# Kernel optimization log

Hardware: AMD Instinct MI355X
Metric: run time of the kernel (lower is better)

The kernel has to match this reference:

```python
import jax, jax.numpy as jnp
import numpy as np

H = 128

def _rnn_layer(inp, W_ih, W_hh, b_ih, b_hh):
    # inp: [B, T, D]; precompute the input projection for all timesteps at once
    pre = jnp.einsum('btd,hd->bth', inp, W_ih) + b_ih + b_hh  # [B, T, H]
    B = inp.shape[0]
    h0 = jnp.zeros((B, H), dtype=inp.dtype)

    def step(h, p_t):  # p_t: [B, H]
        h_new = jnp.tanh(p_t + h @ W_hh.T)
        return h_new, h_new

    _, hs = jax.lax.scan(step, h0, jnp.swapaxes(pre, 0, 1))  # [T, B, H]
    return jnp.swapaxes(hs, 0, 1)  # [B, T, H]


def setup_inputs() -> dict:
    key = jax.random.key(0)
    ks = jax.random.split(key, 12)
    B, T, D = 64, 512, 2048
    s_in = 1.0 / np.sqrt(H)  # PyTorch RNN init scale ~ U(-1/sqrt(H), 1/sqrt(H))
    u = lambda k, shape: jax.random.uniform(k, shape, jnp.float32, -s_in, s_in)
    return {
        'x': jax.random.normal(ks[0], (B, T, D), jnp.float32),
        'W_ih1': u(ks[1], (H, D)),
        'W_hh1': u(ks[2], (H, H)),
        'b_ih1': u(ks[3], (H,)),
        'b_hh1': u(ks[4], (H,)),
        'W_ih2': u(ks[5], (H, H)),
        'W_hh2': u(ks[6], (H, H)),
        'b_ih2': u(ks[7], (H,)),
        'b_hh2': u(ks[8], (H,)),
        'W_fc': u(ks[9], (1, H)),
        'b_fc': u(ks[10], (1,)),
    }


def reference(x, W_ih1, W_hh1, b_ih1, b_hh1, W_ih2, W_hh2, b_ih2, b_hh2, W_fc, b_fc):
    h1 = _rnn_layer(x, W_ih1, W_hh1, b_ih1, b_hh1)   # [B, T, H]
    h2 = _rnn_layer(h1, W_ih2, W_hh2, b_ih2, b_hh2)  # [B, T, H]
    last = h2[:, -1, :]                               # [B, H]
    return last @ W_fc.T + b_fc                       # [B, 1]
```

## Files before the change

### kernel.cpp

```cpp
#include <hip/hip_runtime.h>
#include <cstddef>
#include <cstdint>

#define BB 64
#define TT 512
#define DD 2048
#define HH 128
#define M1 (BB*TT)

typedef __attribute__((ext_vector_type(8))) short bf16x8;
typedef __attribute__((ext_vector_type(4))) float f32x4;
typedef __attribute__((ext_vector_type(2))) _Float16 h2f;

__device__ __forceinline__ unsigned short f2bf(float f) {
    unsigned u = __builtin_bit_cast(unsigned, f);
    u += 0x7fffu + ((u >> 16) & 1u);
    return (unsigned short)(u >> 16);
}
__device__ __forceinline__ float bf2f(unsigned short s) {
    return __builtin_bit_cast(float, ((unsigned)s) << 16);
}
__device__ __forceinline__ float tanh_fast(float x) {
    float e2x = __builtin_amdgcn_exp2f(x * 2.885390081777927f);
    return 1.0f - 2.0f * __builtin_amdgcn_rcpf(e2x + 1.0f);
}

__global__ __launch_bounds__(256) void prep_w_kernel(
    const float* __restrict__ W,
    unsigned short* __restrict__ Whi, unsigned short* __restrict__ Wlo)
{
    const int i = (blockIdx.x * 256 + threadIdx.x) * 4;
    float4 w = *(const float4*)(W + i);
    unsigned short h0 = f2bf(w.x), h1 = f2bf(w.y), h2 = f2bf(w.z), h3 = f2bf(w.w);
    unsigned short l0 = f2bf(w.x - bf2f(h0)), l1 = f2bf(w.y - bf2f(h1));
    unsigned short l2 = f2bf(w.z - bf2f(h2)), l3 = f2bf(w.w - bf2f(h3));
    ushort4 hv; hv.x = h0; hv.y = h1; hv.z = h2; hv.w = h3;
    ushort4 lv; lv.x = l0; lv.y = l1; lv.z = l2; lv.w = l3;
    *(ushort4*)(Whi + i) = hv;
    *(ushort4*)(Wlo + i) = lv;
}

__global__ __launch_bounds__(256) void gemm1_mfma_kernel(
    const float* __restrict__ A, const unsigned short* __restrict__ Whi,
    const unsigned short* __restrict__ Wlo,
    const float* __restrict__ bia, const float* __restrict__ bib,
    float* __restrict__ out)
{
    constexpr int K = DD, BK = 32, NK = K / BK;
    __shared__ __align__(16) short Ah[64 * 40];
    __shared__ __align__(16) short Al[64 * 40];
    __shared__ __align__(16) short Wh[128 * 40];
    __shared__ __align__(16) short Wl[128 * 40];

    const int tid = threadIdx.x, wave = tid >> 6, lane = tid & 63;
    const size_t m0 = (size_t)blockIdx.x * 64;
    const int ar = tid >> 2, ak = (tid & 3) * 8;
    const int wr = tid >> 1, wk = (tid & 1) * 16;
    const float* Ap = A + (m0 + ar) * (size_t)K + ak;
    const unsigned short* Whp = Whi + (size_t)wr * K + wk;
    const unsigned short* Wlp = Wlo + (size_t)wr * K + wk;
    const int frow = lane & 15, fko = (lane >> 4) * 8;

    f32x4 acc[8];
#pragma unroll
    for (int i = 0; i < 8; i++) acc[i] = (f32x4){0.f, 0.f, 0.f, 0.f};

    for (int kt = 0; kt < NK; ++kt) {
        float4 a0 = *(const float4*)(Ap + kt * BK);
        float4 a1 = *(const float4*)(Ap + kt * BK + 4);
        bf16x8 wh0 = *(const bf16x8*)(Whp + kt * BK);
        bf16x8 wh1 = *(const bf16x8*)(Whp + kt * BK + 8);
        bf16x8 wl0 = *(const bf16x8*)(Wlp + kt * BK);
        bf16x8 wl1 = *(const bf16x8*)(Wlp + kt * BK + 8);
        __syncthreads();
        float fv[8] = {a0.x, a0.y, a0.z, a0.w, a1.x, a1.y, a1.z, a1.w};
        unsigned short h[8], l[8];
#pragma unroll
        for (int i = 0; i < 8; i++) {
            h[i] = f2bf(fv[i]);
            l[i] = f2bf(fv[i] - bf2f(h[i]));
        }
        uint2 p0, p1, q0, q1;
        p0.x = (unsigned)h[0] | ((unsigned)h[1] << 16); p0.y = (unsigned)h[2] | ((unsigned)h[3] << 16);
        p1.x = (unsigned)h[4] | ((unsigned)h[5] << 16); p1.y = (unsigned)h[6] | ((unsigned)h[7] << 16);
        q0.x = (unsigned)l[0] | ((unsigned)l[1] << 16); q0.y = (unsigned)l[2] | ((unsigned)l[3] << 16);
        q1.x = (unsigned)l[4] | ((unsigned)l[5] << 16); q1.y = (unsigned)l[6] | ((unsigned)l[7] << 16);
        *(uint2*)&Ah[ar * 40 + ak]     = p0;
        *(uint2*)&Ah[ar * 40 + ak + 4] = p1;
        *(uint2*)&Al[ar * 40 + ak]     = q0;
        *(uint2*)&Al[ar * 40 + ak + 4] = q1;
        *(bf16x8*)&Wh[wr * 40 + wk]     = wh0;
        *(bf16x8*)&Wh[wr * 40 + wk + 8] = wh1;
        *(bf16x8*)&Wl[wr * 40 + wk]     = wl0;
        *(bf16x8*)&Wl[wr * 40 + wk + 8] = wl1;
        __syncthreads();
        bf16x8 fAh = *(const bf16x8*)&Ah[(wave * 16 + frow) * 40 + fko];
        bf16x8 fAl = *(const bf16x8*)&Al[(wave * 16 + frow) * 40 + fko];
#pragma unroll
        for (int nt = 0; nt < 8; ++nt) {
            bf16x8 fWh = *(const bf16x8*)&Wh[(nt * 16 + frow) * 40 + fko];
            bf16x8 fWl = *(const bf16x8*)&Wl[(nt * 16 + frow) * 40 + fko];
            acc[nt] = __builtin_amdgcn_mfma_f32_16x16x32_bf16(fAh, fWh, acc[nt], 0, 0, 0);
            acc[nt] = __builtin_amdgcn_mfma_f32_16x16x32_bf16(fAh, fWl, acc[nt], 0, 0, 0);
            acc[nt] = __builtin_amdgcn_mfma_f32_16x16x32_bf16(fAl, fWh, acc[nt], 0, 0, 0);
        }
    }
    const int rbase = (lane >> 4) * 4;
#pragma unroll
    for (int nt = 0; nt < 8; ++nt) {
        const int col = nt * 16 + frow;
        const float bv = bia[col] + bib[col];
#pragma unroll
        for (int r = 0; r < 4; r++)
            out[(m0 + wave * 16 + rbase + r) * HH + col] = acc[nt][r] + bv;
    }
}

__global__ __launch_bounds__(256, 1) void rnn_scan4_fused1(
    const float* __restrict__ pre,
    const float* __restrict__ Whh,
    const float* __restrict__ Wih2,
    const float* __restrict__ bi2, const float* __restrict__ bh2,
    float* __restrict__ pre2)
{
    __shared__ __align__(16) _Float16 hs[2][HH];
    const int tid  = threadIdx.x;
    const int wave = tid >> 6, lane = tid & 63;
    const int j  = wave * 32 + (lane & 31);
    const int kh = lane >> 5;
    const int b  = blockIdx.x;

    h2f Wr[32];
    h2f W2r[32];
    {
        const float* r = Whh + (size_t)j * HH + kh * 64;
        const float* r2 = Wih2 + (size_t)j * HH + kh * 64;
#pragma unroll
        for (int q = 0; q < 16; q++) {
            float4 w = *(const float4*)(r + q * 4);
            Wr[2 * q]     = h2f{(_Float16)w.x, (_Float16)w.y};
            Wr[2 * q + 1] = h2f{(_Float16)w.z, (_Float16)w.w};
            float4 v = *(const float4*)(r2 + q * 4);
            W2r[2 * q]     = h2f{(_Float16)v.x, (_Float16)v.y};
            W2r[2 * q + 1] = h2f{(_Float16)v.z, (_Float16)v.w};
        }
    }
    const float bias2 = bi2[j] + bh2[j];
    if (tid < HH) hs[0][tid] = (_Float16)0.f;

    const float* pb = pre + (size_t)b * TT * HH;
    float* p2b = pre2 + (size_t)b * TT * HH;
    float pn0 = pb[j];
    float pn1 = pb[(size_t)HH + j];
    __syncthreads();

    for (int t = 0; t < TT; ++t) {
        const float p = pn0;
        pn0 = pn1;
        if (t + 2 < TT) pn1 = pb[(size_t)(t + 2) * HH + j];
        const int rb = t & 1;
        const int wb = rb ^ 1;
        const _Float16* hp = &hs[rb][kh * 64];
        float a0 = 0.f, a1 = 0.f, a2 = 0.f, a3 = 0.f;
#pragma unroll
        for (int q = 0; q < 8; q++) {
            uint4 hv = *(const uint4*)(hp + q * 8);
            h2f x0 = __builtin_bit_cast(h2f, hv.x);
            h2f x1 = __builtin_bit_cast(h2f, hv.y);
            h2f x2 = __builtin_bit_cast(h2f, hv.z);
            h2f x3 = __builtin_bit_cast(h2f, hv.w);
            a0 = __builtin_amdgcn_fdot2(Wr[4 * q],     x0, a0, false);
            a1 = __builtin_amdgcn_fdot2(Wr[4 * q + 1], x1, a1, false);
            a2 = __builtin_amdgcn_fdot2(Wr[4 * q + 2], x2, a2, false);
            a3 = __builtin_amdgcn_fdot2(Wr[4 * q + 3], x3, a3, false);
        }
        float s = (a0 + a1) + (a2 + a3);
        s += __shfl_xor(s, 32);
        const float h = tanh_fast(p + s);
        if (lane < 32) hs[wb][j] = (_Float16)h;
        __syncthreads();

        const _Float16* h2p = &hs[wb][kh * 64];
        float c0 = 0.f, c1 = 0.f, c2 = 0.f, c3 = 0.f;
#pragma unroll
        for (int q = 0; q < 8; q++) {
            uint4 hv = *(const uint4*)(h2p + q * 8);
            h2f x0 = __builtin_bit_cast(h2f, hv.x);
            h2f x1 = __builtin_bit_cast(h2f, hv.y);
            h2f x2 = __builtin_bit_cast(h2f, hv.z);
            h2f x3 = __builtin_bit_cast(h2f, hv.w);
            c0 = __builtin_amdgcn_fdot2(W2r[4 * q],     x0, c0, false);
            c1 = __builtin_amdgcn_fdot2(W2r[4 * q + 1], x1, c1, false);
            c2 = __builtin_amdgcn_fdot2(W2r[4 * q + 2], x2, c2, false);
            c3 = __builtin_amdgcn_fdot2(W2r[4 * q + 3], x3, c3, false);
        }
        float s2 = (c0 + c1) + (c2 + c3);
        s2 += __shfl_xor(s2, 32);
        if (lane < 32) p2b[(size_t)t * HH + j] = s2 + bias2;
    }
}

__global__ __launch_bounds__(256, 1) void rnn_scan4_final(
    const float* __restrict__ pre,
    const float* __restrict__ Whh,
    const float* __restrict__ Wfc, const float* __restrict__ bfc,
    float* __restrict__ outv)
{
    __shared__ __align__(16) _Float16 hs[2][HH];
    __shared__ float red[4];
    const int tid  = threadIdx.x;
    const int wave = tid >> 6, lane = tid & 63;
    const int j  = wave * 32 + (lane & 31);
    const int kh = lane >> 5;
    const int b  = blockIdx.x;

    h2f Wr[32];
    {
        const float* r = Whh + (size_t)j * HH + kh * 64;
#pragma unroll
        for (int q = 0; q < 16; q++) {
            float4 w = *(const float4*)(r + q * 4);
            Wr[2 * q]     = h2f{(_Float16)w.x, (_Float16)w.y};
            Wr[2 * q + 1] = h2f{(_Float16)w.z, (_Float16)w.w};
        }
    }
    if (tid < HH) hs[0][tid] = (_Float16)0.f;

    const float* pb = pre + (size_t)b * TT * HH;
    float pn0 = pb[j];
    float pn1 = pb[(size_t)HH + j];
    float fcv = 0.f;
    __syncthreads();

    for (int t = 0; t < TT; ++t) {
        const float p = pn0;
        pn0 = pn1;
        if (t + 2 < TT) pn1 = pb[(size_t)(t + 2) * HH + j];
        const int rb = t & 1;
        const int wb = rb ^ 1;
        const _Float16* hp = &hs[rb][kh * 64];
        float a0 = 0.f, a1 = 0.f, a2 = 0.f, a3 = 0.f;
#pragma unroll
        for (int q = 0; q < 8; q++) {
            uint4 hv = *(const uint4*)(hp + q * 8);
            h2f x0 = __builtin_bit_cast(h2f, hv.x);
            h2f x1 = __builtin_bit_cast(h2f, hv.y);
            h2f x2 = __builtin_bit_cast(h2f, hv.z);
            h2f x3 = __builtin_bit_cast(h2f, hv.w);
            a0 = __builtin_amdgcn_fdot2(Wr[4 * q],     x0, a0, false);
            a1 = __builtin_amdgcn_fdot2(Wr[4 * q + 1], x1, a1, false);
            a2 = __builtin_amdgcn_fdot2(Wr[4 * q + 2], x2, a2, false);
            a3 = __builtin_amdgcn_fdot2(Wr[4 * q + 3], x3, a3, false);
        }
        float s = (a0 + a1) + (a2 + a3);
        s += __shfl_xor(s, 32);
        const float h = tanh_fast(p + s);
        if (lane < 32) hs[wb][j] = (_Float16)h;
        if (t == TT - 1 && lane < 32) fcv = h * Wfc[j];
        __syncthreads();
    }

#pragma unroll
    for (int off = 1; off < 64; off <<= 1) fcv += __shfl_xor(fcv, off);
    if (lane == 0) red[wave] = fcv;
    __syncthreads();
    if (tid == 0) outv[b] = red[0] + red[1] + red[2] + red[3] + bfc[0];
}

extern "C" void kernel_launch(void* const* d_in, const int* in_sizes, int n_in,
                              void* d_out, int out_size, void* d_ws, size_t ws_size,
                              hipStream_t stream) {
    const float* x    = (const float*)d_in[0];
    const float* Wih1 = (const float*)d_in[1];
    const float* Whh1 = (const float*)d_in[2];
    const float* bih1 = (const float*)d_in[3];
    const float* bhh1 = (const float*)d_in[4];
    const float* Wih2 = (const float*)d_in[5];
    const float* Whh2 = (const float*)d_in[6];
    const float* bih2 = (const float*)d_in[7];
    const float* bhh2 = (const float*)d_in[8];
    const float* Wfc  = (const float*)d_in[9];
    const float* bfc  = (const float*)d_in[10];
    float* out = (float*)d_out;

    float* preA = (float*)d_ws;
    float* preB = preA + (size_t)M1 * HH;
    unsigned short* Whi = (unsigned short*)preB;
    unsigned short* Wlo = Whi + (size_t)HH * DD;

    prep_w_kernel<<<dim3(HH * DD / 1024), dim3(256), 0, stream>>>(Wih1, Whi, Wlo);
    gemm1_mfma_kernel<<<dim3(M1 / 64), dim3(256), 0, stream>>>(x, Whi, Wlo, bih1, bhh1, preA);
    rnn_scan4_fused1<<<dim3(BB), dim3(256), 0, stream>>>(
        preA, Whh1, Wih2, bih2, bhh2, preB);
    rnn_scan4_final<<<dim3(BB), dim3(256), 0, stream>>>(
        preB, Whh2, Wfc, bfc, out);
}
```

Baseline: 882.8 us.

## Split fused scan into producer and consumer waves for layer-2 projection

The fused layer-1 kernel now runs 8 waves per block. Four waves perform the recurrent scan, and four compute the layer-2 input projection for the previous timestep in parallel. This removes the second serial dot product and the extra barrier from each step's critical path, at the cost of a doubled block size and a one-step skew with a tail step after the loop. Weight loading is moved into a helper with an asm register pin so the weights stay resident in registers. The launch bounds no longer force one block per CU.

```diff
diff --git a/kernel.cpp b/kernel.cpp
--- a/kernel.cpp
+++ b/kernel.cpp
@@ -23,6 +23,38 @@
 __device__ __forceinline__ float tanh_fast(float x) {
     float e2x = __builtin_amdgcn_exp2f(x * 2.885390081777927f);
     return 1.0f - 2.0f * __builtin_amdgcn_rcpf(e2x + 1.0f);
+}
+
+__device__ __forceinline__ float dot64_f16(const h2f* Wr, const _Float16* hp) {
+    float a0 = 0.f, a1 = 0.f, a2 = 0.f, a3 = 0.f;
+#pragma unroll
+    for (int q = 0; q < 8; q++) {
+        uint4 hv = *(const uint4*)(hp + q * 8);
+        h2f x0 = __builtin_bit_cast(h2f, hv.x);
+        h2f x1 = __builtin_bit_cast(h2f, hv.y);
+        h2f x2 = __builtin_bit_cast(h2f, hv.z);
+        h2f x3 = __builtin_bit_cast(h2f, hv.w);
+        a0 = __builtin_amdgcn_fdot2(Wr[4 * q],     x0, a0, false);
+        a1 = __builtin_amdgcn_fdot2(Wr[4 * q + 1], x1, a1, false);
+        a2 = __builtin_amdgcn_fdot2(Wr[4 * q + 2], x2, a2, false);
+        a3 = __builtin_amdgcn_fdot2(Wr[4 * q + 3], x3, a3, false);
+    }
+    return (a0 + a1) + (a2 + a3);
+}
+
+__device__ __forceinline__ void load_w32(h2f* Wr, const float* r) {
+#pragma unroll
+    for (int q = 0; q < 16; q++) {
+        float4 w = *(const float4*)(r + q * 4);
+        Wr[2 * q]     = h2f{(_Float16)w.x, (_Float16)w.y};
+        Wr[2 * q + 1] = h2f{(_Float16)w.z, (_Float16)w.w};
+    }
+#pragma unroll
+    for (int i = 0; i < 32; i++) {
+        unsigned u = __builtin_bit_cast(unsigned, Wr[i]);
+        asm volatile("" : "+v"(u));
+        Wr[i] = __builtin_bit_cast(h2f, u);
+    }
 }
 
 __global__ __launch_bounds__(256) void prep_w_kernel(
@@ -116,7 +148,7 @@
     }
 }
 
-__global__ __launch_bounds__(256, 1) void rnn_scan4_fused1(
+__global__ __launch_bounds__(512) void rnn_scan8_fused1(
     const float* __restrict__ pre,
     const float* __restrict__ Whh,
     const float* __restrict__ Wih2,
@@ -126,81 +158,52 @@
     __shared__ __align__(16) _Float16 hs[2][HH];
     const int tid  = threadIdx.x;
     const int wave = tid >> 6, lane = tid & 63;
-    const int j  = wave * 32 + (lane & 31);
+    const int is_scan = (wave < 4);
+    const int j  = (wave & 3) * 32 + (lane & 31);
     const int kh = lane >> 5;
     const int b  = blockIdx.x;
 
     h2f Wr[32];
-    h2f W2r[32];
-    {
-        const float* r = Whh + (size_t)j * HH + kh * 64;
-        const float* r2 = Wih2 + (size_t)j * HH + kh * 64;
-#pragma unroll
-        for (int q = 0; q < 16; q++) {
-            float4 w = *(const float4*)(r + q * 4);
-            Wr[2 * q]     = h2f{(_Float16)w.x, (_Float16)w.y};
-            Wr[2 * q + 1] = h2f{(_Float16)w.z, (_Float16)w.w};
-            float4 v = *(const float4*)(r2 + q * 4);
-            W2r[2 * q]     = h2f{(_Float16)v.x, (_Float16)v.y};
-            W2r[2 * q + 1] = h2f{(_Float16)v.z, (_Float16)v.w};
-        }
-    }
-    const float bias2 = bi2[j] + bh2[j];
+    load_w32(Wr, (is_scan ? Whh : Wih2) + (size_t)j * HH + kh * 64);
+    float bias2 = 0.f;
+    if (!is_scan) bias2 = bi2[j] + bh2[j];
     if (tid < HH) hs[0][tid] = (_Float16)0.f;
 
     const float* pb = pre + (size_t)b * TT * HH;
     float* p2b = pre2 + (size_t)b * TT * HH;
-    float pn0 = pb[j];
-    float pn1 = pb[(size_t)HH + j];
+    float pn0 = 0.f, pn1 = 0.f;
+    if (is_scan) {
+        pn0 = pb[j];
+        pn1 = pb[(size_t)HH + j];
+    }
     __syncthreads();
 
     for (int t = 0; t < TT; ++t) {
-        const float p = pn0;
-        pn0 = pn1;
-        if (t + 2 < TT) pn1 = pb[(size_t)(t + 2) * HH + j];
         const int rb = t & 1;
         const int wb = rb ^ 1;
-        const _Float16* hp = &hs[rb][kh * 64];
-        float a0 = 0.f, a1 = 0.f, a2 = 0.f, a3 = 0.f;
-#pragma unroll
-        for (int q = 0; q < 8; q++) {
-            uint4 hv = *(const uint4*)(hp + q * 8);
-            h2f x0 = __builtin_bit_cast(h2f, hv.x);
-            h2f x1 = __builtin_bit_cast(h2f, hv.y);
-            h2f x2 = __builtin_bit_cast(h2f, hv.z);
-            h2f x3 = __builtin_bit_cast(h2f, hv.w);
-            a0 = __builtin_amdgcn_fdot2(Wr[4 * q],     x0, a0, false);
-            a1 = __builtin_amdgcn_fdot2(Wr[4 * q + 1], x1, a1, false);
-            a2 = __builtin_amdgcn_fdot2(Wr[4 * q + 2], x2, a2, false);
-            a3 = __builtin_amdgcn_fdot2(Wr[4 * q + 3], x3, a3, false);
+        if (is_scan) {
+            const float p = pn0;
+            pn0 = pn1;
+            if (t + 2 < TT) pn1 = pb[(size_t)(t + 2) * HH + j];
+            float s = dot64_f16(Wr, &hs[rb][kh * 64]);
+            s += __shfl_xor(s, 32);
+            const float h = tanh_fast(p + s);
+            if (lane < 32) hs[wb][j] = (_Float16)h;
+        } else if (t > 0) {
+            float s2 = dot64_f16(Wr, &hs[rb][kh * 64]);
+            s2 += __shfl_xor(s2, 32);
+            if (lane < 32) p2b[(size_t)(t - 1) * HH + j] = s2 + bias2;
         }
-        float s = (a0 + a1) + (a2 + a3);
-        s += __shfl_xor(s, 32);
-        const float h = tanh_fast(p + s);
-        if (lane < 32) hs[wb][j] = (_Float16)h;
-        __syncthreads();
-
-        const _Float16* h2p = &hs[wb][kh * 64];
-        float c0 = 0.f, c1 = 0.f, c2 = 0.f, c3 = 0.f;
-#pragma unroll
-        for (int q = 0; q < 8; q++) {
-            uint4 hv = *(const uint4*)(h2p + q * 8);
-            h2f x0 = __builtin_bit_cast(h2f, hv.x);
-            h2f x1 = __builtin_bit_cast(h2f, hv.y);
-            h2f x2 = __builtin_bit_cast(h2f, hv.z);
-            h2f x3 = __builtin_bit_cast(h2f, hv.w);
-            c0 = __builtin_amdgcn_fdot2(W2r[4 * q],     x0, c0, false);
-            c1 = __builtin_amdgcn_fdot2(W2r[4 * q + 1], x1, c1, false);
-            c2 = __builtin_amdgcn_fdot2(W2r[4 * q + 2], x2, c2, false);
-            c3 = __builtin_amdgcn_fdot2(W2r[4 * q + 3], x3, c3, false);
-        }
-        float s2 = (c0 + c1) + (c2 + c3);
+        __syncthreads();
+    }
+    if (!is_scan) {
+        float s2 = dot64_f16(Wr, &hs[TT & 1][kh * 64]);
         s2 += __shfl_xor(s2, 32);
-        if (lane < 32) p2b[(size_t)t * HH + j] = s2 + bias2;
-    }
-}
-
-__global__ __launch_bounds__(256, 1) void rnn_scan4_final(
+        if (lane < 32) p2b[(size_t)(TT - 1) * HH + j] = s2 + bias2;
+    }
+}
+
+__global__ __launch_bounds__(256) void rnn_scan4_final(
     const float* __restrict__ pre,
     const float* __restrict__ Whh,
     const float* __restrict__ Wfc, const float* __restrict__ bfc,
@@ -215,15 +218,7 @@
     const int b  = blockIdx.x;
 
     h2f Wr[32];
-    {
-        const float* r = Whh + (size_t)j * HH + kh * 64;
-#pragma unroll
-        for (int q = 0; q < 16; q++) {
-            float4 w = *(const float4*)(r + q * 4);
-            Wr[2 * q]     = h2f{(_Float16)w.x, (_Float16)w.y};
-            Wr[2 * q + 1] = h2f{(_Float16)w.z, (_Float16)w.w};
-        }
-    }
+    load_w32(Wr, Whh + (size_t)j * HH + kh * 64);
     if (tid < HH) hs[0][tid] = (_Float16)0.f;
 
     const float* pb = pre + (size_t)b * TT * HH;
@@ -238,21 +233,7 @@
         if (t + 2 < TT) pn1 = pb[(size_t)(t + 2) * HH + j];
         const int rb = t & 1;
         const int wb = rb ^ 1;
-        const _Float16* hp = &hs[rb][kh * 64];
-        float a0 = 0.f, a1 = 0.f, a2 = 0.f, a3 = 0.f;
-#pragma unroll
-        for (int q = 0; q < 8; q++) {
-            uint4 hv = *(const uint4*)(hp + q * 8);
-            h2f x0 = __builtin_bit_cast(h2f, hv.x);
-            h2f x1 = __builtin_bit_cast(h2f, hv.y);
-            h2f x2 = __builtin_bit_cast(h2f, hv.z);
-            h2f x3 = __builtin_bit_cast(h2f, hv.w);
-            a0 = __builtin_amdgcn_fdot2(Wr[4 * q],     x0, a0, false);
-            a1 = __builtin_amdgcn_fdot2(Wr[4 * q + 1], x1, a1, false);
-            a2 = __builtin_amdgcn_fdot2(Wr[4 * q + 2], x2, a2, false);
-            a3 = __builtin_amdgcn_fdot2(Wr[4 * q + 3], x3, a3, false);
-        }
-        float s = (a0 + a1) + (a2 + a3);
+        float s = dot64_f16(Wr, &hs[rb][kh * 64]);
         s += __shfl_xor(s, 32);
         const float h = tanh_fast(p + s);
         if (lane < 32) hs[wb][j] = (_Float16)h;
@@ -290,7 +271,7 @@
 
     prep_w_kernel<<<dim3(HH * DD / 1024), dim3(256), 0, stream>>>(Wih1, Whi, Wlo);
     gemm1_mfma_kernel<<<dim3(M1 / 64), dim3(256), 0, stream>>>(x, Whi, Wlo, bih1, bhh1, preA);
-    rnn_scan4_fused1<<<dim3(BB), dim3(256), 0, stream>>>(
+    rnn_scan8_fused1<<<dim3(BB), dim3(512), 0, stream>>>(
         preA, Whh1, Wih2, bih2, bhh2, preB);
     rnn_scan4_final<<<dim3(BB), dim3(256), 0, stream>>>(
         preB, Whh2, Wfc, bfc, out);
```

Result: faster. 762.0 us (-13.7%).
